# Performance work log

Measured on AMD Instinct MI355X. Metric: run time of the kernel, lower is better.

## Reference

```python
import jax, jax.numpy as jnp
import numpy as np
from jax import lax

INPUT_SIZE, HIDDEN, NUM_LAYERS, NUM_CLASSES = 22, 10, 2, 4
B, T = 1024, 1000


def _run_layer(seq, w_ih, w_hh, b_ih, b_hh):
    # seq: (T, B, F_in) -> (T, B, H); Elman RNN with ReLU nonlinearity
    h0 = jnp.zeros((seq.shape[1], w_hh.shape[0]), seq.dtype)
    def step(h, x_t):
        h_new = jax.nn.relu(x_t @ w_ih.T + h @ w_hh.T + (b_ih + b_hh))
        return h_new, h_new
    _, hs = lax.scan(step, h0, seq)
    return hs


def setup_inputs() -> dict:
    key = jax.random.key(0)
    ks = jax.random.split(key, 12)
    s = 1.0 / np.sqrt(HIDDEN)  # torch nn.RNN init scale
    u = lambda k, shape: jax.random.uniform(k, shape, jnp.float32, -s, s)
    return {
        "x": jax.random.normal(ks[0], (B, T, INPUT_SIZE), jnp.float32),
        "w_ih0": u(ks[1], (HIDDEN, INPUT_SIZE)),
        "w_hh0": u(ks[2], (HIDDEN, HIDDEN)),
        "b_ih0": u(ks[3], (HIDDEN,)),
        "b_hh0": u(ks[4], (HIDDEN,)),
        "w_ih1": u(ks[5], (HIDDEN, HIDDEN)),
        "w_hh1": u(ks[6], (HIDDEN, HIDDEN)),
        "b_ih1": u(ks[7], (HIDDEN,)),
        "b_hh1": u(ks[8], (HIDDEN,)),
        "w_lin": u(ks[9], (NUM_CLASSES, HIDDEN)),
        "b_lin": u(ks[10], (NUM_CLASSES,)),
    }


def reference(x, w_ih0, w_hh0, b_ih0, b_hh0, w_ih1, w_hh1, b_ih1, b_hh1, w_lin, b_lin):
    seq = jnp.transpose(x, (1, 0, 2))                      # (T, B, F)
    h1 = _run_layer(seq, w_ih0, w_hh0, b_ih0, b_hh0)       # (T, B, H)
    h2 = _run_layer(h1, w_ih1, w_hh1, b_ih1, b_hh1)        # (T, B, H)
    last = jax.nn.relu(h2[-1])                             # (B, H)
    return last @ w_lin.T + b_lin                          # (B, num_classes)
```

## Files before the change

### kernel.cpp

```cpp
#include <hip/hip_runtime.h>

typedef float v2f __attribute__((ext_vector_type(2)));
typedef _Float16 h2f __attribute__((ext_vector_type(2)));

namespace {

constexpr int Tn = 1000, Fn = 22, Hn = 10, Cn = 4;
constexpr int CHF = 32 * Fn;

__device__ __forceinline__ v2f mk2(float a, float b){ v2f r; r.x=a; r.y=b; return r; }
__device__ __forceinline__ v2f fma2(v2f a, v2f b, v2f c){ return __builtin_elementwise_fma(a,b,c); }
__device__ __forceinline__ float rlanef(float v, int l){
    return __uint_as_float(__builtin_amdgcn_readlane(__float_as_uint(v), l));
}
__device__ __forceinline__ unsigned rlaneu(unsigned v, int l){
    return (unsigned)__builtin_amdgcn_readlane((int)v, l);
}
__device__ __forceinline__ void gld_lds4(const float* g, float* l){
    __builtin_amdgcn_global_load_lds(
        (const __attribute__((address_space(1))) unsigned int*)g,
        (__attribute__((address_space(3))) unsigned int*)l, 4, 0, 0);
}
__device__ __forceinline__ void sfence(){ __builtin_amdgcn_sched_barrier(0); }
__device__ __forceinline__ h2f u2h(unsigned u){ return __builtin_bit_cast(h2f, u); }

__global__ __launch_bounds__(64, 1) void rnn_dot16(
    const float* __restrict__ x,
    const float* __restrict__ w_ih0, const float* __restrict__ w_hh0,
    const float* __restrict__ b_ih0, const float* __restrict__ b_hh0,
    const float* __restrict__ w_ih1, const float* __restrict__ w_hh1,
    const float* __restrict__ b_ih1, const float* __restrict__ b_hh1,
    const float* __restrict__ w_lin, const float* __restrict__ b_lin,
    float* __restrict__ out)
{
    __shared__ __align__(16) float ch[2][CHF];

    const int lane = threadIdx.x;
    const int b    = blockIdx.x;
    const int half = lane >> 5;
    const int l31  = lane & 31;

    const int jz = (l31 < Hn) ? l31 : 0;
    const bool isl2 = (l31 >= 16) && (l31 < 16 + Hn);
    const int j2 = isl2 ? (l31 - 16) : 0;

    const float* pwa = (l31 < 16) ? (w_hh0 + jz * Hn) : (w_ih1 + j2 * Hn);
    h2f waH[5], wbH[5];
    #pragma unroll
    for (int k = 0; k < 5; ++k) {
        h2f t; t.x = (_Float16)pwa[2*k]; t.y = (_Float16)pwa[2*k+1];
        waH[k] = t;
        h2f u; u.x = isl2 ? (_Float16)w_hh1[j2*Hn + 2*k]     : (_Float16)0.f;
               u.y = isl2 ? (_Float16)w_hh1[j2*Hn + 2*k + 1] : (_Float16)0.f;
        wbH[k] = u;
    }
    v2f wih0p[11];
    #pragma unroll
    for (int p = 0; p < 11; ++p)
        wih0p[p] = mk2(w_ih0[jz*Fn + 2*p], w_ih0[jz*Fn + 2*p + 1]);
    const float bias1  = b_ih0[jz] + b_hh0[jz];
    const float bias2v = b_ih1[j2] + b_hh1[j2];
    const v2f bz2 = mk2(bias1, 0.f);

    const bool mL = (lane < Hn);
    const bool mU = (lane >= 32) && (lane < 32+Hn);

    const float* __restrict__ xrow = x + (size_t)b * (Tn * Fn);

    auto stage = [&](int c) {
        float* dst = ch[c & 1];
        const float* src = xrow + c * CHF;
        if (c < 31) {
            #pragma unroll
            for (int k = 0; k < 11; ++k) gld_lds4(src + k*64 + lane, dst + k*64);
        } else {
            gld_lds4(src + lane, dst);
            gld_lds4(src + 64 + lane, dst + 64);
            if (lane < 48) gld_lds4(src + 128 + lane, dst + 128);
        }
    };
    stage(0); stage(1);

    v2f xd[11], xv0[11], xv1[11];
    {
        const float* r01 = xrow + half * Fn;
        #pragma unroll
        for (int p = 0; p < 11; ++p) xd[p] = *(const v2f*)(r01 + 2*p);
        const float* r23 = xrow + (2 + half) * Fn;
        #pragma unroll
        for (int p = 0; p < 11; ++p) xv0[p] = *(const v2f*)(r23 + 2*p);
    }

    auto zc = [&](const v2f* xp) -> float {
        v2f z = fma2(xp[0], wih0p[0], bz2);
        #pragma unroll
        for (int p = 1; p < 11; ++p) z = fma2(xp[p], wih0p[p], z);
        return z.x + z.y;
    };
    auto pairptr = [&](int P) -> const float* {
        return &ch[(P >> 4) & 1][(P & 15) * 44 + half * 22];
    };
    auto loadxv = [&](v2f* dst, const float* rp) {
        #pragma unroll
        for (int p = 0; p < 11; ++p) dst[p] = *(const v2f*)(rp + 2*p);
        sfence();
    };

    unsigned S1u[5], S2u[5];
    #pragma unroll
    for (int k = 0; k < 5; ++k) { S1u[k] = 0u; S2u[k] = 0u; }

    float zA, zB;
    asm volatile("s_waitcnt vmcnt(0)" ::: "memory");
    zA = zc(xd);

    auto dostep = [&](bool up, float z, bool commit2) {
        const float base = (up ? mU : mL) ? z : bias2v;
        float aA = base, aB = 0.f;
        #pragma unroll
        for (int k = 0; k < 5; ++k)
            aA = __builtin_amdgcn_fdot2(u2h(S1u[k]), waH[k], aA, false);
        #pragma unroll
        for (int k = 0; k < 5; ++k)
            aB = __builtin_amdgcn_fdot2(u2h(S2u[k]), wbH[k], aB, false);
        const float hn = fmaxf(aA + aB, 0.f);
        const float nb = __uint_as_float((unsigned)__builtin_amdgcn_mov_dpp(
                             (int)__float_as_uint(hn), 0xB1, 0xF, 0xF, false));
        const unsigned pk = __builtin_bit_cast(unsigned,
                             __builtin_amdgcn_cvt_pkrtz(hn, nb));
        const int s1b = up ? 32 : 0;
        #pragma unroll
        for (int k = 0; k < 5; ++k) S1u[k] = rlaneu(pk, s1b + 2*k);
        if (commit2) {
            #pragma unroll
            for (int k = 0; k < 5; ++k) S2u[k] = rlaneu(pk, s1b + 16 + 2*k);
        }
    };

    auto MACRO = [&](int m, bool s2_0, bool ld0, bool ld1, bool z1) {
        if (ld0) loadxv(xv1, pairptr(2*m + 2));
        dostep(false, zA, s2_0);
        zB = zc(xv0);
        dostep(true, zA, true);
        if (ld1) loadxv(xv0, pairptr(2*m + 3));
        dostep(false, zB, true);
        if (z1) zA = zc(xv1);
        dostep(true, zB, true);
    };

    MACRO(0, false, true, true, true);

    #pragma unroll 1
    for (int m = 1; m < 249; ++m) {
        if ((m & 7) == 7) {
            asm volatile("s_waitcnt vmcnt(0)" ::: "memory");
            const int c = (m >> 3) + 2;
            if (c <= 31) stage(c);
        }
        MACRO(m, true, true, true, true);
    }
    MACRO(249, true, false, false, false);

    float S2f[Hn];
    {
        float aA = bias2v, aB = 0.f;
        #pragma unroll
        for (int k = 0; k < 5; ++k)
            aA = __builtin_amdgcn_fdot2(u2h(S1u[k]), waH[k], aA, false);
        #pragma unroll
        for (int k = 0; k < 5; ++k)
            aB = __builtin_amdgcn_fdot2(u2h(S2u[k]), wbH[k], aB, false);
        const float h2f_ = fmaxf(aA + aB, 0.f);
        #pragma unroll
        for (int k = 0; k < Hn; ++k) S2f[k] = rlanef(h2f_, 16 + k);
    }

    const int jc = (lane < Cn) ? lane : 0;
    float o = b_lin[jc];
    #pragma unroll
    for (int k = 0; k < Hn; ++k) o = fmaf(S2f[k], w_lin[jc*Hn + k], o);
    if (lane < Cn) out[b * Cn + lane] = o;
}

}

extern "C" void kernel_launch(void* const* d_in, const int* in_sizes, int n_in,
                              void* d_out, int out_size, void* d_ws, size_t ws_size,
                              hipStream_t stream) {
    const float* x     = (const float*)d_in[0];
    const float* w_ih0 = (const float*)d_in[1];
    const float* w_hh0 = (const float*)d_in[2];
    const float* b_ih0 = (const float*)d_in[3];
    const float* b_hh0 = (const float*)d_in[4];
    const float* w_ih1 = (const float*)d_in[5];
    const float* w_hh1 = (const float*)d_in[6];
    const float* b_ih1 = (const float*)d_in[7];
    const float* b_hh1 = (const float*)d_in[8];
    const float* w_lin = (const float*)d_in[9];
    const float* b_lin = (const float*)d_in[10];
    float* out = (float*)d_out;

    rnn_dot16<<<dim3(1024), dim3(64), 0, stream>>>(
        x, w_ih0, w_hh0, b_ih0, b_hh0,
        w_ih1, w_hh1, b_ih1, b_hh1, w_lin, b_lin, out);
}
```

Before: 104.0 us.

## Split RNN layers across two wavefronts with LDS handoff and chunk-lagged pipeline

Layer 1 now runs in wave 0, which writes packed fp16 hidden states to a double-buffered LDS ring. Wave 1 runs layer 2 one chunk behind, reading those states back. Before, one wave computed both layers in lockstep with a combined dot-product chain and cross-layer readlanes. The split shortens each wave's per-step serial dependency chain and lets the two layers overlap, at the cost of a block barrier per chunk and twice the threads per block.

```diff
diff --git a/kernel.cpp b/kernel.cpp
--- a/kernel.cpp
+++ b/kernel.cpp
@@ -7,12 +7,13 @@
 
 constexpr int Tn = 1000, Fn = 22, Hn = 10, Cn = 4;
 constexpr int CHF = 32 * Fn;
+constexpr int XZ  = 2 * CHF;
+constexpr int RZ  = XZ;
+constexpr int DZ  = XZ + 512;
+constexpr int LDSF = DZ + 576;
 
 __device__ __forceinline__ v2f mk2(float a, float b){ v2f r; r.x=a; r.y=b; return r; }
 __device__ __forceinline__ v2f fma2(v2f a, v2f b, v2f c){ return __builtin_elementwise_fma(a,b,c); }
-__device__ __forceinline__ float rlanef(float v, int l){
-    return __uint_as_float(__builtin_amdgcn_readlane(__float_as_uint(v), l));
-}
 __device__ __forceinline__ unsigned rlaneu(unsigned v, int l){
     return (unsigned)__builtin_amdgcn_readlane((int)v, l);
 }
@@ -22,9 +23,18 @@
         (__attribute__((address_space(3))) unsigned int*)l, 4, 0, 0);
 }
 __device__ __forceinline__ void sfence(){ __builtin_amdgcn_sched_barrier(0); }
+__device__ __forceinline__ void lgkm0_bar(){
+    asm volatile("s_waitcnt lgkmcnt(0)" ::: "memory");
+    __builtin_amdgcn_s_barrier();
+}
 __device__ __forceinline__ h2f u2h(unsigned u){ return __builtin_bit_cast(h2f, u); }
-
-__global__ __launch_bounds__(64, 1) void rnn_dot16(
+__device__ __forceinline__ unsigned packpair(float hn){
+    const float nb = __uint_as_float((unsigned)__builtin_amdgcn_mov_dpp(
+                         (int)__float_as_uint(hn), 0xB1, 0xF, 0xF, false));
+    return __builtin_bit_cast(unsigned, __builtin_amdgcn_cvt_pkrtz(hn, nb));
+}
+
+__global__ __launch_bounds__(128, 2) void rnn_lag(
     const float* __restrict__ x,
     const float* __restrict__ w_ih0, const float* __restrict__ w_hh0,
     const float* __restrict__ b_ih0, const float* __restrict__ b_hh0,
@@ -33,153 +43,210 @@
     const float* __restrict__ w_lin, const float* __restrict__ b_lin,
     float* __restrict__ out)
 {
-    __shared__ __align__(16) float ch[2][CHF];
-
-    const int lane = threadIdx.x;
+    __shared__ __align__(16) float lds[LDSF];
+
+    const int tid  = threadIdx.x;
+    const int wid  = tid >> 6;
+    const int lane = tid & 63;
     const int b    = blockIdx.x;
-    const int half = lane >> 5;
-    const int l31  = lane & 31;
-
-    const int jz = (l31 < Hn) ? l31 : 0;
-    const bool isl2 = (l31 >= 16) && (l31 < 16 + Hn);
-    const int j2 = isl2 ? (l31 - 16) : 0;
-
-    const float* pwa = (l31 < 16) ? (w_hh0 + jz * Hn) : (w_ih1 + j2 * Hn);
-    h2f waH[5], wbH[5];
-    #pragma unroll
-    for (int k = 0; k < 5; ++k) {
-        h2f t; t.x = (_Float16)pwa[2*k]; t.y = (_Float16)pwa[2*k+1];
-        waH[k] = t;
-        h2f u; u.x = isl2 ? (_Float16)w_hh1[j2*Hn + 2*k]     : (_Float16)0.f;
-               u.y = isl2 ? (_Float16)w_hh1[j2*Hn + 2*k + 1] : (_Float16)0.f;
-        wbH[k] = u;
+    const float* __restrict__ xrow = x + (size_t)b * (Tn * Fn);
+
+    if (wid == 0) {
+        const int half = lane >> 5;
+        const int l31  = lane & 31;
+        const int jz   = (l31 < Hn) ? l31 : 0;
+
+        h2f waH[5];
+        #pragma unroll
+        for (int k = 0; k < 5; ++k) {
+            h2f t; t.x = (_Float16)w_hh0[jz*Hn + 2*k];
+                   t.y = (_Float16)w_hh0[jz*Hn + 2*k + 1];
+            waH[k] = t;
+        }
+        v2f wih0p[11];
+        #pragma unroll
+        for (int p = 0; p < 11; ++p)
+            wih0p[p] = mk2(w_ih0[jz*Fn + 2*p], w_ih0[jz*Fn + 2*p + 1]);
+        const v2f bz2 = mk2(b_ih0[jz] + b_hh0[jz], 0.f);
+
+        const bool vE = (lane < 10) && !(lane & 1);
+        const bool vO = (lane >= 32) && (lane < 42) && !(lane & 1);
+        const int wEi = vE ? RZ + (lane >> 1)        : DZ + lane;
+        const int wOi = vO ? RZ + ((lane - 32) >> 1) : DZ + lane;
+
+        auto stage = [&](int c) {
+            float* dst = lds + (c & 1) * CHF;
+            const float* src = xrow + c * CHF;
+            if (c < 31) {
+                #pragma unroll
+                for (int k = 0; k < 11; ++k) gld_lds4(src + k*64 + lane, dst + k*64);
+            } else {
+                gld_lds4(src + lane, dst);
+                gld_lds4(src + 64 + lane, dst + 64);
+                if (lane < 48) gld_lds4(src + 128 + lane, dst + 128);
+            }
+        };
+        stage(0); stage(1);
+
+        v2f xd[11], xv0[11], xv1[11];
+        {
+            const float* r01 = xrow + half * Fn;
+            #pragma unroll
+            for (int p = 0; p < 11; ++p) xd[p] = *(const v2f*)(r01 + 2*p);
+            const float* r23 = xrow + (2 + half) * Fn;
+            #pragma unroll
+            for (int p = 0; p < 11; ++p) xv0[p] = *(const v2f*)(r23 + 2*p);
+        }
+        auto zc = [&](const v2f* xp) -> float {
+            v2f z = fma2(xp[0], wih0p[0], bz2);
+            #pragma unroll
+            for (int p = 1; p < 11; ++p) z = fma2(xp[p], wih0p[p], z);
+            return z.x + z.y;
+        };
+        auto loadxv = [&](v2f* dst, const float* rp) {
+            #pragma unroll
+            for (int p = 0; p < 11; ++p) dst[p] = *(const v2f*)(rp + 2*p);
+            sfence();
+        };
+
+        unsigned S1u[5];
+        #pragma unroll
+        for (int k = 0; k < 5; ++k) S1u[k] = 0u;
+
+        asm volatile("s_waitcnt vmcnt(0)" ::: "memory");
+        float zA = zc(xd), zB;
+
+        auto stepA = [&](float z, int rbase, float* wp, int stoff) {
+            float c0 = __builtin_amdgcn_fdot2(u2h(S1u[0]), waH[0], z, false);
+            c0 = __builtin_amdgcn_fdot2(u2h(S1u[1]), waH[1], c0, false);
+            c0 = __builtin_amdgcn_fdot2(u2h(S1u[2]), waH[2], c0, false);
+            float c1 = __builtin_amdgcn_fdot2(u2h(S1u[3]), waH[3], 0.f, false);
+            c1 = __builtin_amdgcn_fdot2(u2h(S1u[4]), waH[4], c1, false);
+            const float hn = fmaxf(c0 + c1, 0.f);
+            const unsigned pk = packpair(hn);
+            #pragma unroll
+            for (int k = 0; k < 5; ++k) S1u[k] = rlaneu(pk, rbase + 2*k);
+            wp[stoff] = __uint_as_float(pk);
+        };
+        auto MACRO = [&](const float* l0, const float* l1,
+                         float* wE, float* wO, int st, bool z1) {
+            if (l0) loadxv(xv1, l0);
+            stepA(zA, 0,  wE, (st + 0) * 8);
+            zB = zc(xv0);
+            stepA(zA, 32, wO, (st + 1) * 8);
+            if (l1) loadxv(xv0, l1);
+            stepA(zB, 0,  wE, (st + 2) * 8);
+            if (z1) zA = zc(xv1);
+            stepA(zB, 32, wO, (st + 3) * 8);
+        };
+
+        #pragma unroll 1
+        for (int s = 0; s <= 32; ++s) {
+            if (s < 32) {
+                const int sh = (s & 1) * 256;
+                float* wE = lds + wEi + sh;
+                float* wO = lds + wOi + sh;
+                const float* xbt = lds + (s & 1) * CHF + half * 22;
+                const float* xbn = lds + ((s + 1) & 1) * CHF + half * 22;
+                if (s < 31) {
+                    #pragma unroll
+                    for (int mm = 0; mm < 7; ++mm)
+                        MACRO(xbt + (2*mm + 2) * 44, xbt + (2*mm + 3) * 44,
+                              wE, wO, mm * 4, true);
+                    asm volatile("s_waitcnt vmcnt(0)" ::: "memory");
+                    if (s + 2 <= 31) stage(s + 2);
+                    MACRO(xbn, xbn + 44, wE, wO, 28, true);
+                } else {
+                    MACRO(xbt + 2*44, xbt + 3*44, wE, wO, 0, true);
+                    MACRO(nullptr, nullptr, wE, wO, 4, false);
+                }
+            }
+            lgkm0_bar();
+        }
+    } else {
+        const int j2 = (lane < Hn) ? lane : 0;
+        h2f wih1H[5], whh1H[5], wlinH[5];
+        const int jc = (lane < Cn) ? lane : 0;
+        #pragma unroll
+        for (int k = 0; k < 5; ++k) {
+            h2f t; t.x = (_Float16)w_ih1[j2*Hn + 2*k];
+                   t.y = (_Float16)w_ih1[j2*Hn + 2*k + 1];
+            wih1H[k] = t;
+            h2f u; u.x = (_Float16)w_hh1[j2*Hn + 2*k];
+                   u.y = (_Float16)w_hh1[j2*Hn + 2*k + 1];
+            whh1H[k] = u;
+            h2f w; w.x = (_Float16)w_lin[jc*Hn + 2*k];
+                   w.y = (_Float16)w_lin[jc*Hn + 2*k + 1];
+            wlinH[k] = w;
+        }
+        const float b2v = b_ih1[j2] + b_hh1[j2];
+        const float blv = b_lin[jc];
+
+        unsigned S2u[5];
+        #pragma unroll
+        for (int k = 0; k < 5; ++k) S2u[k] = 0u;
+
+        auto stepB = [&](uint4 q, unsigned q4) {
+            float d0 = __builtin_amdgcn_fdot2(u2h(q.x), wih1H[0], b2v, false);
+            d0 = __builtin_amdgcn_fdot2(u2h(q.y), wih1H[1], d0, false);
+            d0 = __builtin_amdgcn_fdot2(u2h(q.z), wih1H[2], d0, false);
+            float d1 = __builtin_amdgcn_fdot2(u2h(q.w), wih1H[3], 0.f, false);
+            d1 = __builtin_amdgcn_fdot2(u2h(q4),  wih1H[4], d1, false);
+            d0 = __builtin_amdgcn_fdot2(u2h(S2u[0]), whh1H[0], d0, false);
+            d1 = __builtin_amdgcn_fdot2(u2h(S2u[1]), whh1H[1], d1, false);
+            d0 = __builtin_amdgcn_fdot2(u2h(S2u[2]), whh1H[2], d0, false);
+            d1 = __builtin_amdgcn_fdot2(u2h(S2u[3]), whh1H[3], d1, false);
+            d0 = __builtin_amdgcn_fdot2(u2h(S2u[4]), whh1H[4], d0, false);
+            const float hn = fmaxf(d0 + d1, 0.f);
+            const unsigned pk = packpair(hn);
+            #pragma unroll
+            for (int k = 0; k < 5; ++k) S2u[k] = rlaneu(pk, 2*k);
+        };
+
+        #pragma unroll 1
+        for (int s = 0; s <= 32; ++s) {
+            if (s >= 1) {
+                const float* rb = lds + RZ + ((s - 1) & 1) * 256;
+                uint4 qa = *(const uint4*)(rb + 0);
+                unsigned ra = *(const unsigned*)(rb + 4);
+                uint4 qb = *(const uint4*)(rb + 8);
+                unsigned rbx = *(const unsigned*)(rb + 12);
+                sfence();
+                if (s - 1 < 31) {
+                    #pragma unroll
+                    for (int st = 0; st < 32; st += 2) {
+                        uint4 ca = qa; unsigned c4a = ra;
+                        if (st + 2 < 32) { qa = *(const uint4*)(rb + (st+2)*8);
+                                           ra = *(const unsigned*)(rb + (st+2)*8 + 4); }
+                        stepB(ca, c4a);
+                        uint4 cb = qb; unsigned c4b = rbx;
+                        if (st + 3 < 32) { qb = *(const uint4*)(rb + (st+3)*8);
+                                           rbx = *(const unsigned*)(rb + (st+3)*8 + 4); }
+                        stepB(cb, c4b);
+                    }
+                } else {
+                    #pragma unroll
+                    for (int st = 0; st < 8; st += 2) {
+                        uint4 ca = qa; unsigned c4a = ra;
+                        if (st + 2 < 8) { qa = *(const uint4*)(rb + (st+2)*8);
+                                          ra = *(const unsigned*)(rb + (st+2)*8 + 4); }
+                        stepB(ca, c4a);
+                        uint4 cb = qb; unsigned c4b = rbx;
+                        if (st + 3 < 8) { qb = *(const uint4*)(rb + (st+3)*8);
+                                          rbx = *(const unsigned*)(rb + (st+3)*8 + 4); }
+                        stepB(cb, c4b);
+                    }
+                }
+            }
+            lgkm0_bar();
+        }
+
+        float o = blv;
+        #pragma unroll
+        for (int k = 0; k < 5; ++k)
+            o = __builtin_amdgcn_fdot2(u2h(S2u[k]), wlinH[k], o, false);
+        if (lane < Cn) out[b * Cn + lane] = o;
     }
-    v2f wih0p[11];
-    #pragma unroll
-    for (int p = 0; p < 11; ++p)
-        wih0p[p] = mk2(w_ih0[jz*Fn + 2*p], w_ih0[jz*Fn + 2*p + 1]);
-    const float bias1  = b_ih0[jz] + b_hh0[jz];
-    const float bias2v = b_ih1[j2] + b_hh1[j2];
-    const v2f bz2 = mk2(bias1, 0.f);
-
-    const bool mL = (lane < Hn);
-    const bool mU = (lane >= 32) && (lane < 32+Hn);
-
-    const float* __restrict__ xrow = x + (size_t)b * (Tn * Fn);
-
-    auto stage = [&](int c) {
-        float* dst = ch[c & 1];
-        const float* src = xrow + c * CHF;
-        if (c < 31) {
-            #pragma unroll
-            for (int k = 0; k < 11; ++k) gld_lds4(src + k*64 + lane, dst + k*64);
-        } else {
-            gld_lds4(src + lane, dst);
-            gld_lds4(src + 64 + lane, dst + 64);
-            if (lane < 48) gld_lds4(src + 128 + lane, dst + 128);
-        }
-    };
-    stage(0); stage(1);
-
-    v2f xd[11], xv0[11], xv1[11];
-    {
-        const float* r01 = xrow + half * Fn;
-        #pragma unroll
-        for (int p = 0; p < 11; ++p) xd[p] = *(const v2f*)(r01 + 2*p);
-        const float* r23 = xrow + (2 + half) * Fn;
-        #pragma unroll
-        for (int p = 0; p < 11; ++p) xv0[p] = *(const v2f*)(r23 + 2*p);
-    }
-
-    auto zc = [&](const v2f* xp) -> float {
-        v2f z = fma2(xp[0], wih0p[0], bz2);
-        #pragma unroll
-        for (int p = 1; p < 11; ++p) z = fma2(xp[p], wih0p[p], z);
-        return z.x + z.y;
-    };
-    auto pairptr = [&](int P) -> const float* {
-        return &ch[(P >> 4) & 1][(P & 15) * 44 + half * 22];
-    };
-    auto loadxv = [&](v2f* dst, const float* rp) {
-        #pragma unroll
-        for (int p = 0; p < 11; ++p) dst[p] = *(const v2f*)(rp + 2*p);
-        sfence();
-    };
-
-    unsigned S1u[5], S2u[5];
-    #pragma unroll
-    for (int k = 0; k < 5; ++k) { S1u[k] = 0u; S2u[k] = 0u; }
-
-    float zA, zB;
-    asm volatile("s_waitcnt vmcnt(0)" ::: "memory");
-    zA = zc(xd);
-
-    auto dostep = [&](bool up, float z, bool commit2) {
-        const float base = (up ? mU : mL) ? z : bias2v;
-        float aA = base, aB = 0.f;
-        #pragma unroll
-        for (int k = 0; k < 5; ++k)
-            aA = __builtin_amdgcn_fdot2(u2h(S1u[k]), waH[k], aA, false);
-        #pragma unroll
-        for (int k = 0; k < 5; ++k)
-            aB = __builtin_amdgcn_fdot2(u2h(S2u[k]), wbH[k], aB, false);
-        const float hn = fmaxf(aA + aB, 0.f);
-        const float nb = __uint_as_float((unsigned)__builtin_amdgcn_mov_dpp(
-                             (int)__float_as_uint(hn), 0xB1, 0xF, 0xF, false));
-        const unsigned pk = __builtin_bit_cast(unsigned,
-                             __builtin_amdgcn_cvt_pkrtz(hn, nb));
-        const int s1b = up ? 32 : 0;
-        #pragma unroll
-        for (int k = 0; k < 5; ++k) S1u[k] = rlaneu(pk, s1b + 2*k);
-        if (commit2) {
-            #pragma unroll
-            for (int k = 0; k < 5; ++k) S2u[k] = rlaneu(pk, s1b + 16 + 2*k);
-        }
-    };
-
-    auto MACRO = [&](int m, bool s2_0, bool ld0, bool ld1, bool z1) {
-        if (ld0) loadxv(xv1, pairptr(2*m + 2));
-        dostep(false, zA, s2_0);
-        zB = zc(xv0);
-        dostep(true, zA, true);
-        if (ld1) loadxv(xv0, pairptr(2*m + 3));
-        dostep(false, zB, true);
-        if (z1) zA = zc(xv1);
-        dostep(true, zB, true);
-    };
-
-    MACRO(0, false, true, true, true);
-
-    #pragma unroll 1
-    for (int m = 1; m < 249; ++m) {
-        if ((m & 7) == 7) {
-            asm volatile("s_waitcnt vmcnt(0)" ::: "memory");
-            const int c = (m >> 3) + 2;
-            if (c <= 31) stage(c);
-        }
-        MACRO(m, true, true, true, true);
-    }
-    MACRO(249, true, false, false, false);
-
-    float S2f[Hn];
-    {
-        float aA = bias2v, aB = 0.f;
-        #pragma unroll
-        for (int k = 0; k < 5; ++k)
-            aA = __builtin_amdgcn_fdot2(u2h(S1u[k]), waH[k], aA, false);
-        #pragma unroll
-        for (int k = 0; k < 5; ++k)
-            aB = __builtin_amdgcn_fdot2(u2h(S2u[k]), wbH[k], aB, false);
-        const float h2f_ = fmaxf(aA + aB, 0.f);
-        #pragma unroll
-        for (int k = 0; k < Hn; ++k) S2f[k] = rlanef(h2f_, 16 + k);
-    }
-
-    const int jc = (lane < Cn) ? lane : 0;
-    float o = b_lin[jc];
-    #pragma unroll
-    for (int k = 0; k < Hn; ++k) o = fmaf(S2f[k], w_lin[jc*Hn + k], o);
-    if (lane < Cn) out[b * Cn + lane] = o;
 }
 
 }
@@ -200,7 +267,7 @@
     const float* b_lin = (const float*)d_in[10];
     float* out = (float*)d_out;
 
-    rnn_dot16<<<dim3(1024), dim3(64), 0, stream>>>(
+    rnn_lag<<<dim3(1024), dim3(128), 0, stream>>>(
         x, w_ih0, w_hh0, b_ih0, b_hh0,
         w_ih1, w_hh1, b_ih1, b_hh1, w_lin, b_lin, out);
 }
```

Result: slower. 118.7 us (+14.1%).

## Precompute layer-0 input projections into LDS before the serial recurrence

Applied to the files above, without the earlier changes.

The kernel is split into two phases. First, all 1000 layer-0 input projections (x·W_ih0 + bias) are computed with all 64 lanes and stored in a 40KB LDS buffer. Then the skewed two-layer recurrence runs on lanes 0-31 only, reading its z values from LDS in batches of eight, with each step's dot products split into four independent fdot2 chains to shorten the dependency chain. The intent is to take the input-projection FMAs and the staged global-to-LDS loads off the per-step critical path. In exchange it adds an up-front serial precompute phase and a large LDS footprint, and the final linear layer now reads fp16 hidden states.

```diff
diff --git a/kernel.cpp b/kernel.cpp
--- a/kernel.cpp
+++ b/kernel.cpp
@@ -6,25 +6,16 @@
 namespace {
 
 constexpr int Tn = 1000, Fn = 22, Hn = 10, Cn = 4;
-constexpr int CHF = 32 * Fn;
 
 __device__ __forceinline__ v2f mk2(float a, float b){ v2f r; r.x=a; r.y=b; return r; }
 __device__ __forceinline__ v2f fma2(v2f a, v2f b, v2f c){ return __builtin_elementwise_fma(a,b,c); }
-__device__ __forceinline__ float rlanef(float v, int l){
-    return __uint_as_float(__builtin_amdgcn_readlane(__float_as_uint(v), l));
-}
 __device__ __forceinline__ unsigned rlaneu(unsigned v, int l){
     return (unsigned)__builtin_amdgcn_readlane((int)v, l);
 }
-__device__ __forceinline__ void gld_lds4(const float* g, float* l){
-    __builtin_amdgcn_global_load_lds(
-        (const __attribute__((address_space(1))) unsigned int*)g,
-        (__attribute__((address_space(3))) unsigned int*)l, 4, 0, 0);
-}
+__device__ __forceinline__ h2f u2h(unsigned u){ return __builtin_bit_cast(h2f, u); }
 __device__ __forceinline__ void sfence(){ __builtin_amdgcn_sched_barrier(0); }
-__device__ __forceinline__ h2f u2h(unsigned u){ return __builtin_bit_cast(h2f, u); }
 
-__global__ __launch_bounds__(64, 1) void rnn_dot16(
+__global__ __launch_bounds__(64, 1) void rnn_zpre(
     const float* __restrict__ x,
     const float* __restrict__ w_ih0, const float* __restrict__ w_hh0,
     const float* __restrict__ b_ih0, const float* __restrict__ b_hh0,
@@ -33,18 +24,64 @@
     const float* __restrict__ w_lin, const float* __restrict__ b_lin,
     float* __restrict__ out)
 {
-    __shared__ __align__(16) float ch[2][CHF];
+    __shared__ float zl[10240];
 
     const int lane = threadIdx.x;
     const int b    = blockIdx.x;
-    const int half = lane >> 5;
-    const int l31  = lane & 31;
+    const float* __restrict__ xb = x + (size_t)b * (Tn * Fn);
 
-    const int jz = (l31 < Hn) ? l31 : 0;
-    const bool isl2 = (l31 >= 16) && (l31 < 16 + Hn);
-    const int j2 = isl2 ? (l31 - 16) : 0;
+    {
+        const int g = lane / 10;
+        const int j = lane - 10 * g;
+        v2f wih[11];
+        #pragma unroll
+        for (int p = 0; p < 11; ++p) wih[p] = *(const v2f*)(w_ih0 + j*Fn + 2*p);
+        const float b1 = b_ih0[j] + b_hh0[j];
 
-    const float* pwa = (l31 < 16) ? (w_hh0 + jz * Hn) : (w_ih1 + j2 * Hn);
+        v2f xr[5][11];
+        auto ldx = [&](v2f* d, int trow){
+            const float* s = xb + trow * Fn;
+            #pragma unroll
+            for (int p = 0; p < 11; ++p) d[p] = *(const v2f*)(s + 2*p);
+        };
+        auto dotz = [&](const v2f* v)->float{
+            v2f a = fma2(v[0], wih[0], mk2(b1, 0.f));
+            #pragma unroll
+            for (int p = 1; p < 11; ++p) a = fma2(v[p], wih[p], a);
+            return a.x + a.y;
+        };
+        #pragma unroll
+        for (int s = 0; s < 5; ++s) ldx(xr[s], g + 6*s);
+
+        auto body = [&](int i, v2f* slot){
+            const float z = dotz(slot);
+            const int zi = lane + 60 * i;
+            if (zi < 10000) zl[zi] = z;
+            int tr = g + 6*i + 30;
+            tr = (tr > 999) ? 999 : tr;
+            ldx(slot, tr);
+        };
+        #pragma unroll 1
+        for (int i = 0; i < 165; i += 5) {
+            body(i,   xr[0]); body(i+1, xr[1]); body(i+2, xr[2]);
+            body(i+3, xr[3]); body(i+4, xr[4]);
+        }
+        { const float z = dotz(xr[0]); const int zi = lane + 60*165; if (zi < 10000) zl[zi] = z; }
+        { const float z = dotz(xr[1]); const int zi = lane + 60*166; if (zi < 10000) zl[zi] = z; }
+
+        #pragma unroll
+        for (int k = 0; k < 4; ++k) {
+            const int idx = 10000 + lane + 64*k;
+            if (idx < 10240) zl[idx] = 0.f;
+        }
+    }
+    asm volatile("s_waitcnt lgkmcnt(0)" ::: "memory");
+
+    const int jz   = (lane < Hn) ? lane : 0;
+    const bool isl2 = (lane >= 16) && (lane < 16 + Hn);
+    const int j2   = isl2 ? (lane - 16) : 0;
+
+    const float* pwa = (lane < 16) ? (w_hh0 + jz*Hn) : (w_ih1 + j2*Hn);
     h2f waH[5], wbH[5];
     #pragma unroll
     for (int k = 0; k < 5; ++k) {
@@ -54,131 +91,77 @@
                u.y = isl2 ? (_Float16)w_hh1[j2*Hn + 2*k + 1] : (_Float16)0.f;
         wbH[k] = u;
     }
-    v2f wih0p[11];
-    #pragma unroll
-    for (int p = 0; p < 11; ++p)
-        wih0p[p] = mk2(w_ih0[jz*Fn + 2*p], w_ih0[jz*Fn + 2*p + 1]);
-    const float bias1  = b_ih0[jz] + b_hh0[jz];
-    const float bias2v = b_ih1[j2] + b_hh1[j2];
-    const v2f bz2 = mk2(bias1, 0.f);
-
-    const bool mL = (lane < Hn);
-    const bool mU = (lane >= 32) && (lane < 32+Hn);
-
-    const float* __restrict__ xrow = x + (size_t)b * (Tn * Fn);
-
-    auto stage = [&](int c) {
-        float* dst = ch[c & 1];
-        const float* src = xrow + c * CHF;
-        if (c < 31) {
-            #pragma unroll
-            for (int k = 0; k < 11; ++k) gld_lds4(src + k*64 + lane, dst + k*64);
-        } else {
-            gld_lds4(src + lane, dst);
-            gld_lds4(src + 64 + lane, dst + 64);
-            if (lane < 48) gld_lds4(src + 128 + lane, dst + 128);
-        }
-    };
-    stage(0); stage(1);
-
-    v2f xd[11], xv0[11], xv1[11];
-    {
-        const float* r01 = xrow + half * Fn;
-        #pragma unroll
-        for (int p = 0; p < 11; ++p) xd[p] = *(const v2f*)(r01 + 2*p);
-        const float* r23 = xrow + (2 + half) * Fn;
-        #pragma unroll
-        for (int p = 0; p < 11; ++p) xv0[p] = *(const v2f*)(r23 + 2*p);
-    }
-
-    auto zc = [&](const v2f* xp) -> float {
-        v2f z = fma2(xp[0], wih0p[0], bz2);
-        #pragma unroll
-        for (int p = 1; p < 11; ++p) z = fma2(xp[p], wih0p[p], z);
-        return z.x + z.y;
-    };
-    auto pairptr = [&](int P) -> const float* {
-        return &ch[(P >> 4) & 1][(P & 15) * 44 + half * 22];
-    };
-    auto loadxv = [&](v2f* dst, const float* rp) {
-        #pragma unroll
-        for (int p = 0; p < 11; ++p) dst[p] = *(const v2f*)(rp + 2*p);
-        sfence();
-    };
+    const float b2v = isl2 ? (b_ih1[j2] + b_hh1[j2]) : 0.f;
 
     unsigned S1u[5], S2u[5];
     #pragma unroll
     for (int k = 0; k < 5; ++k) { S1u[k] = 0u; S2u[k] = 0u; }
 
-    float zA, zB;
-    asm volatile("s_waitcnt vmcnt(0)" ::: "memory");
-    zA = zc(xd);
+    const float* zp = zl + ((lane < Hn) ? (10 + lane) : 10000);
+    const int zinc  = (lane < Hn) ? 160 : 0;
 
-    auto dostep = [&](bool up, float z, bool commit2) {
-        const float base = (up ? mU : mL) ? z : bias2v;
-        float aA = base, aB = 0.f;
-        #pragma unroll
-        for (int k = 0; k < 5; ++k)
-            aA = __builtin_amdgcn_fdot2(u2h(S1u[k]), waH[k], aA, false);
-        #pragma unroll
-        for (int k = 0; k < 5; ++k)
-            aB = __builtin_amdgcn_fdot2(u2h(S2u[k]), wbH[k], aB, false);
-        const float hn = fmaxf(aA + aB, 0.f);
-        const float nb = __uint_as_float((unsigned)__builtin_amdgcn_mov_dpp(
-                             (int)__float_as_uint(hn), 0xB1, 0xF, 0xF, false));
+    auto stepc = [&](float zc, bool c2) {
+        float c0 = __builtin_amdgcn_fdot2(u2h(S1u[0]), waH[0], zc, false);
+        c0 = __builtin_amdgcn_fdot2(u2h(S1u[1]), waH[1], c0, false);
+        c0 = __builtin_amdgcn_fdot2(u2h(S1u[2]), waH[2], c0, false);
+        float c1 = __builtin_amdgcn_fdot2(u2h(S1u[3]), waH[3], 0.f, false);
+        c1 = __builtin_amdgcn_fdot2(u2h(S1u[4]), waH[4], c1, false);
+        float c2a = __builtin_amdgcn_fdot2(u2h(S2u[0]), wbH[0], b2v, false);
+        c2a = __builtin_amdgcn_fdot2(u2h(S2u[1]), wbH[1], c2a, false);
+        c2a = __builtin_amdgcn_fdot2(u2h(S2u[2]), wbH[2], c2a, false);
+        float c3 = __builtin_amdgcn_fdot2(u2h(S2u[3]), wbH[3], 0.f, false);
+        c3 = __builtin_amdgcn_fdot2(u2h(S2u[4]), wbH[4], c3, false);
+        const float s = (c0 + c1) + (c2a + c3);
+        const float sw = __uint_as_float((unsigned)__builtin_amdgcn_mov_dpp(
+                             (int)__float_as_uint(s), 0xB1, 0xF, 0xF, false));
+        const float lo = fmaxf(s, 0.f);
+        const float hi = fmaxf(sw, 0.f);
         const unsigned pk = __builtin_bit_cast(unsigned,
-                             __builtin_amdgcn_cvt_pkrtz(hn, nb));
-        const int s1b = up ? 32 : 0;
-        #pragma unroll
-        for (int k = 0; k < 5; ++k) S1u[k] = rlaneu(pk, s1b + 2*k);
-        if (commit2) {
-            #pragma unroll
-            for (int k = 0; k < 5; ++k) S2u[k] = rlaneu(pk, s1b + 16 + 2*k);
+                             __builtin_amdgcn_cvt_pkrtz(lo, hi));
+        S1u[0] = rlaneu(pk, 0);  S1u[1] = rlaneu(pk, 2);
+        S1u[2] = rlaneu(pk, 4);  S1u[3] = rlaneu(pk, 6);
+        S1u[4] = rlaneu(pk, 8);
+        if (c2) {
+            S2u[0] = rlaneu(pk, 16); S2u[1] = rlaneu(pk, 18);
+            S2u[2] = rlaneu(pk, 20); S2u[3] = rlaneu(pk, 22);
+            S2u[4] = rlaneu(pk, 24);
         }
     };
 
-    auto MACRO = [&](int m, bool s2_0, bool ld0, bool ld1, bool z1) {
-        if (ld0) loadxv(xv1, pairptr(2*m + 2));
-        dostep(false, zA, s2_0);
-        zB = zc(xv0);
-        dostep(true, zA, true);
-        if (ld1) loadxv(xv0, pairptr(2*m + 3));
-        dostep(false, zB, true);
-        if (z1) zA = zc(xv1);
-        dostep(true, zB, true);
-    };
+    { const float z0 = zl[(lane < Hn) ? lane : 10000]; stepc(z0, false); }
 
-    MACRO(0, false, true, true, true);
+    float za[8], zb[8];
+    #pragma unroll
+    for (int s = 0; s < 8; ++s) za[s] = zp[10*s];
 
     #pragma unroll 1
-    for (int m = 1; m < 249; ++m) {
-        if ((m & 7) == 7) {
-            asm volatile("s_waitcnt vmcnt(0)" ::: "memory");
-            const int c = (m >> 3) + 2;
-            if (c <= 31) stage(c);
-        }
-        MACRO(m, true, true, true, true);
+    for (int it = 0; it < 62; ++it) {
+        #pragma unroll
+        for (int s = 0; s < 8; ++s) zb[s] = zp[80 + 10*s];
+        sfence();
+        #pragma unroll
+        for (int s = 0; s < 8; ++s) stepc(za[s], true);
+        #pragma unroll
+        for (int s = 0; s < 8; ++s) za[s] = zp[160 + 10*s];
+        sfence();
+        #pragma unroll
+        for (int s = 0; s < 8; ++s) stepc(zb[s], true);
+        zp += zinc;
     }
-    MACRO(249, true, false, false, false);
-
-    float S2f[Hn];
-    {
-        float aA = bias2v, aB = 0.f;
-        #pragma unroll
-        for (int k = 0; k < 5; ++k)
-            aA = __builtin_amdgcn_fdot2(u2h(S1u[k]), waH[k], aA, false);
-        #pragma unroll
-        for (int k = 0; k < 5; ++k)
-            aB = __builtin_amdgcn_fdot2(u2h(S2u[k]), wbH[k], aB, false);
-        const float h2f_ = fmaxf(aA + aB, 0.f);
-        #pragma unroll
-        for (int k = 0; k < Hn; ++k) S2f[k] = rlanef(h2f_, 16 + k);
-    }
+    #pragma unroll
+    for (int s = 0; s < 8; ++s) stepc(za[s], true);
 
     const int jc = (lane < Cn) ? lane : 0;
+    h2f wlinH[5];
+    #pragma unroll
+    for (int k = 0; k < 5; ++k) {
+        h2f w; w.x = (_Float16)w_lin[jc*Hn + 2*k]; w.y = (_Float16)w_lin[jc*Hn + 2*k + 1];
+        wlinH[k] = w;
+    }
     float o = b_lin[jc];
     #pragma unroll
-    for (int k = 0; k < Hn; ++k) o = fmaf(S2f[k], w_lin[jc*Hn + k], o);
+    for (int k = 0; k < 5; ++k)
+        o = __builtin_amdgcn_fdot2(u2h(S2u[k]), wlinH[k], o, false);
     if (lane < Cn) out[b * Cn + lane] = o;
 }
 
@@ -200,7 +183,7 @@
     const float* b_lin = (const float*)d_in[10];
     float* out = (float*)d_out;
 
-    rnn_dot16<<<dim3(1024), dim3(64), 0, stream>>>(
+    rnn_zpre<<<dim3(1024), dim3(64), 0, stream>>>(
         x, w_ih0, w_hh0, b_ih0, b_hh0,
         w_ih1, w_hh1, b_ih1, b_hh1, w_lin, b_lin, out);
 }
```

Result: no change. 103.2 us (-0.7%).
